# Kernel optimization log

Measured on AMD Instinct MI355X. Metric: run time of the kernel, lower is better.

## Reference

```python
import jax, jax.numpy as jnp
import numpy as np

DIM = 1024
NUM_HEADS = 16


def setup_inputs() -> dict:
    key = jax.random.key(0)
    ks = jax.random.split(key, 6)
    B, N, C = 2, 2048, DIM
    x = jax.random.normal(ks[0], (B, N, C), dtype=jnp.float32)
    # torch nn.Linear weights have shape (out, in); qkv_bias=False, proj has bias
    wq = jax.random.normal(ks[1], (C, C), dtype=jnp.float32) * 0.02
    wk = jax.random.normal(ks[2], (C, C), dtype=jnp.float32) * 0.02
    wv = jax.random.normal(ks[3], (C, C), dtype=jnp.float32) * 0.02
    wp = jax.random.normal(ks[4], (C, C), dtype=jnp.float32) * 0.02
    bp = jax.random.normal(ks[5], (C,), dtype=jnp.float32) * 0.02
    return {"x": x, "wq": wq, "wk": wk, "wv": wv, "wp": wp, "bp": bp}


def reference(x, wq, wk, wv, wp, bp):
    B, N, C = x.shape
    H = NUM_HEADS
    D = C // H
    scale = D ** (-0.5)
    # projections (torch Linear: x @ W.T), split heads -> (B, H, N, D)
    q = (x @ wq.T).reshape(B, N, H, D).transpose(0, 2, 1, 3)
    k = (x @ wk.T).reshape(B, N, H, D).transpose(0, 2, 1, 3)
    v = (x @ wv.T).reshape(B, N, H, D).transpose(0, 2, 1, 3)
    # average keys over sequence -> (B, H, D)
    k_avg = k.mean(axis=2)
    # per-position logits against the single averaged key -> (B, H, N)
    z = jnp.einsum('bhnd,bhd->bhn', q, k_avg) * scale
    attn = jax.nn.softmax(z, axis=-1)  # (B, H, N); dropout is identity at eval
    # build circulant matrix: roll_weights[..., i, j] = attn[..., (j - i) mod N]
    pos = jnp.arange(N)
    idx = (pos[None, :] - pos[:, None]) % N  # (N, N)
    roll_weights = attn[:, :, idx]  # (B, H, N, N) gather-built circulant
    out = jnp.einsum('bhij,bhjd->bhid', roll_weights, v)  # (B, H, N, D)
    out = out.transpose(0, 2, 1, 3).reshape(B, N, C)
    return out @ wp.T + bp
```

## Files before the change

### kernel.cpp

```cpp
#include <hip/hip_runtime.h>
#include <stdint.h>

typedef unsigned short u16;
typedef __bf16 bf16x8 __attribute__((ext_vector_type(8)));
typedef float f32x4 __attribute__((ext_vector_type(4)));

static constexpr int kDim   = 1024;
static constexpr int kHeads = 16;
static constexpr int kN     = 2048;
static constexpr int kB     = 2;
static constexpr int kTok   = 4096;

static constexpr size_t OFF_XB   = 0;
static constexpr size_t OFF_VT   = OFF_XB   + (size_t)kTok*kDim*2;
static constexpr size_t OFF_OC   = OFF_VT   + (size_t)kTok*kDim*2;
static constexpr size_t OFF_WVB  = OFF_OC   + (size_t)kTok*kDim*2;
static constexpr size_t OFF_WPB  = OFF_WVB  + (size_t)kDim*kDim*2;
static constexpr size_t OFF_XSUM = OFF_WPB  + (size_t)kDim*kDim*2;
static constexpr size_t OFF_KAVG = OFF_XSUM + (size_t)kB*kDim*4;
static constexpr size_t OFF_WZ   = OFF_KAVG + (size_t)kB*kHeads*64*4;
static constexpr size_t OFF_Z    = OFF_WZ   + (size_t)kB*kHeads*kDim*4;
static constexpr size_t OFF_ATTN = OFF_Z    + (size_t)kB*kHeads*kN*4;
static constexpr int kAttnStride = 2064;

__device__ __forceinline__ u16 f2bf(float f) {
  unsigned int u = __builtin_bit_cast(unsigned int, f);
  u = (u + 0x7FFFu + ((u >> 16) & 1u)) >> 16;
  return (u16)u;
}

__device__ __forceinline__ void gload_lds16(const void* g, void* l) {
  __builtin_amdgcn_global_load_lds(
      (const __attribute__((address_space(1))) unsigned int*)g,
      (__attribute__((address_space(3))) unsigned int*)l, 16, 0, 0);
}

__global__ void cvt_bf16_kernel(const float* __restrict__ in, u16* __restrict__ out, int n4) {
  int i = blockIdx.x * 256 + threadIdx.x;
  if (i < n4) {
    float4 f = reinterpret_cast<const float4*>(in)[i];
    u16 a = f2bf(f.x), b = f2bf(f.y), c = f2bf(f.z), d = f2bf(f.w);
    unsigned int lo = (unsigned int)a | ((unsigned int)b << 16);
    unsigned int hi = (unsigned int)c | ((unsigned int)d << 16);
    reinterpret_cast<uint2*>(out)[i] = make_uint2(lo, hi);
  }
}

__global__ void xsum_kernel(const float* __restrict__ x, float* __restrict__ xsum) {
  int bid = blockIdx.x;
  int cc = bid & 3, nc = (bid >> 2) & 15, b = bid >> 6;
  int c = cc * 256 + threadIdx.x;
  const float* xp = x + ((size_t)b * kN + nc * 128) * kDim + c;
  float s = 0.f;
  for (int n = 0; n < 128; ++n) s += xp[(size_t)n * kDim];
  atomicAdd(&xsum[b * kDim + c], s);
}

__global__ void kavg_kernel(const float* __restrict__ xsum, const float* __restrict__ wk,
                            float* __restrict__ kavg) {
  int o = blockIdx.x;
  int b = o >> 10;
  int lane = threadIdx.x;
  const float* wkr = wk + (size_t)(o & 1023) * kDim;
  const float* xs = xsum + b * kDim;
  float s = 0.f;
  for (int k = lane; k < kDim; k += 64) s += xs[k] * wkr[k];
#pragma unroll
  for (int off = 32; off; off >>= 1) s += __shfl_xor(s, off);
  if (lane == 0) kavg[o] = s * (1.0f / (float)kN);
}

__global__ void wz_kernel(const float* __restrict__ kavg, const float* __restrict__ wq,
                          float* __restrict__ wz) {
  int bh = blockIdx.x;
  int h = bh & 15, tid = threadIdx.x;
  __shared__ float kl[64];
  if (tid < 64) kl[tid] = kavg[bh * 64 + tid];
  __syncthreads();
  float a0 = 0.f, a1 = 0.f, a2 = 0.f, a3 = 0.f;
  const float* wqb = wq + (size_t)h * 64 * kDim + tid;
  for (int d = 0; d < 64; ++d) {
    float kd = kl[d];
    const float* r = wqb + (size_t)d * kDim;
    a0 += kd * r[0]; a1 += kd * r[256]; a2 += kd * r[512]; a3 += kd * r[768];
  }
  const float scale = 0.125f;
  float* o = wz + (size_t)bh * kDim + tid;
  o[0] = a0 * scale; o[256] = a1 * scale; o[512] = a2 * scale; o[768] = a3 * scale;
}

__global__ void z_kernel(const float* __restrict__ x, const float* __restrict__ wz,
                         float* __restrict__ z) {
  int blk = blockIdx.x;
  int b = blk >> 11, n = blk & 2047;
  __shared__ float xr[kDim];
  int tid = threadIdx.x, wid = tid >> 6, lane = tid & 63;
  reinterpret_cast<float4*>(xr)[tid] = reinterpret_cast<const float4*>(x + (size_t)blk * kDim)[tid];
  __syncthreads();
#pragma unroll
  for (int hh = 0; hh < 4; ++hh) {
    int h = wid * 4 + hh;
    const float* wzr = wz + (size_t)(b * kHeads + h) * kDim;
    float s = 0.f;
    for (int k = lane; k < kDim; k += 64) s += xr[k] * wzr[k];
#pragma unroll
    for (int off = 32; off; off >>= 1) s += __shfl_xor(s, off);
    if (lane == 0) z[(size_t)(b * kHeads + h) * kN + n] = s;
  }
}

__global__ void softmax_kernel(const float* __restrict__ z, u16* __restrict__ attn2) {
  int row = blockIdx.x, tid = threadIdx.x;
  int lane = tid & 63, wid = tid >> 6;
  const float* zr = z + (size_t)row * kN;
  float v[8];
  float mx = -1e30f;
#pragma unroll
  for (int j = 0; j < 8; ++j) { v[j] = zr[tid + j * 256]; mx = fmaxf(mx, v[j]); }
#pragma unroll
  for (int off = 32; off; off >>= 1) mx = fmaxf(mx, __shfl_xor(mx, off));
  __shared__ float redm[4], reds[4];
  if (lane == 0) redm[wid] = mx;
  __syncthreads();
  mx = fmaxf(fmaxf(redm[0], redm[1]), fmaxf(redm[2], redm[3]));
  float s = 0.f;
#pragma unroll
  for (int j = 0; j < 8; ++j) { v[j] = __expf(v[j] - mx); s += v[j]; }
#pragma unroll
  for (int off = 32; off; off >>= 1) s += __shfl_xor(s, off);
  if (lane == 0) reds[wid] = s;
  __syncthreads();
  s = reds[0] + reds[1] + reds[2] + reds[3];
  float inv = 1.0f / s;
  u16* out = attn2 + (size_t)row * kAttnStride;
#pragma unroll
  for (int j = 0; j < 8; ++j) out[tid + j * 256] = f2bf(v[j] * inv);
  if (tid < 8) out[2048 + tid] = f2bf(v[0] * inv);
}

template <int MODE>
__global__ __launch_bounds__(256, 2)
void gemm_bt_kernel(const u16* __restrict__ A, const u16* __restrict__ B,
                    void* __restrict__ Cout, const float* __restrict__ bias, int K) {
  __shared__ __align__(16) u16 As[128 * 64];
  __shared__ __align__(16) u16 Bs[64 * 64];
  int tid = threadIdx.x, lane = tid & 63, wid = tid >> 6;
  int wm = wid >> 1, wn = wid & 1;
  int lrow = lane & 15, kg = lane >> 4;
  int m0 = blockIdx.y * 128, n0 = blockIdx.x * 64;

  f32x4 acc[4][2];
#pragma unroll
  for (int i = 0; i < 4; ++i)
#pragma unroll
    for (int j = 0; j < 2; ++j) acc[i][j] = (f32x4){0.f, 0.f, 0.f, 0.f};

  for (int k0 = 0; k0 < K; k0 += 64) {
#pragma unroll
    for (int it = 0; it < 4; ++it) {
      int bchunk = it * 256 + wid * 64;
      int chunk = bchunk + lane;
      int row = chunk >> 3, cb = chunk & 7;
      int cs = cb ^ (row & 7);
      gload_lds16(A + (size_t)(m0 + row) * K + k0 + cs * 8, &As[bchunk * 8]);
    }
#pragma unroll
    for (int it = 0; it < 2; ++it) {
      int bchunk = it * 256 + wid * 64;
      int chunk = bchunk + lane;
      int row = chunk >> 3, cb = chunk & 7;
      int cs = cb ^ (row & 7);
      gload_lds16(B + (size_t)(n0 + row) * K + k0 + cs * 8, &Bs[bchunk * 8]);
    }
    __syncthreads();
#pragma unroll
    for (int ks = 0; ks < 2; ++ks) {
      bf16x8 af[4], bfv[2];
#pragma unroll
      for (int mf = 0; mf < 4; ++mf) {
        int r = wm * 64 + mf * 16 + lrow;
        int c = (ks * 4 + kg) ^ (r & 7);
        af[mf] = *reinterpret_cast<const bf16x8*>(&As[r * 64 + c * 8]);
      }
#pragma unroll
      for (int nf = 0; nf < 2; ++nf) {
        int r = wn * 32 + nf * 16 + lrow;
        int c = (ks * 4 + kg) ^ (r & 7);
        bfv[nf] = *reinterpret_cast<const bf16x8*>(&Bs[r * 64 + c * 8]);
      }
#pragma unroll
      for (int mf = 0; mf < 4; ++mf)
#pragma unroll
        for (int nf = 0; nf < 2; ++nf)
          acc[mf][nf] = __builtin_amdgcn_mfma_f32_16x16x32_bf16(af[mf], bfv[nf], acc[mf][nf], 0, 0, 0);
    }
    __syncthreads();
  }

  if (MODE == 0) {
    u16* vT = (u16*)Cout;
#pragma unroll
    for (int mf = 0; mf < 4; ++mf) {
      int row0 = m0 + wm * 64 + mf * 16 + kg * 4;
      int bb = row0 >> 11, u = row0 & 2047;
#pragma unroll
      for (int nf = 0; nf < 2; ++nf) {
        int col = n0 + wn * 32 + nf * 16 + lrow;
        f32x4 a = acc[mf][nf];
        unsigned int lo = (unsigned int)f2bf(a.x) | ((unsigned int)f2bf(a.y) << 16);
        unsigned int hi = (unsigned int)f2bf(a.z) | ((unsigned int)f2bf(a.w) << 16);
        *reinterpret_cast<uint2*>(&vT[((size_t)(bb * kDim + col)) * kN + u]) = make_uint2(lo, hi);
      }
    }
  } else {
    float* y = (float*)Cout;
#pragma unroll
    for (int nf = 0; nf < 2; ++nf) {
      int col = n0 + wn * 32 + nf * 16 + lrow;
      float bv = bias[col];
#pragma unroll
      for (int mf = 0; mf < 4; ++mf) {
        int row0 = m0 + wm * 64 + mf * 16 + kg * 4;
        f32x4 a = acc[mf][nf];
        y[(size_t)(row0 + 0) * kDim + col] = a.x + bv;
        y[(size_t)(row0 + 1) * kDim + col] = a.y + bv;
        y[(size_t)(row0 + 2) * kDim + col] = a.z + bv;
        y[(size_t)(row0 + 3) * kDim + col] = a.w + bv;
      }
    }
  }
}

__global__ __launch_bounds__(256, 2)
void conv_kernel(const u16* __restrict__ vT, const u16* __restrict__ attn2,
                 u16* __restrict__ oc) {
  static constexpr int RS = 2056;
  __shared__ __align__(16) u16 reps[8 * RS];
  __shared__ __align__(16) u16 vts[64 * 64];
  int tid = threadIdx.x, lane = tid & 63, wid = tid >> 6;
  int wm = wid >> 1, wn = wid & 1;
  int lrow = lane & 15, kg = lane >> 4;
  int i0 = blockIdx.x * 128;
  int bh = blockIdx.y;
  int b = bh >> 4, h = bh & 15;

  const u16* arow = attn2 + (size_t)bh * kAttnStride;
  for (int p = 0; p < 8; ++p)
    for (int j = tid; j < 2048; j += 256) reps[p * RS + j] = arow[j + p];

  f32x4 acc[2][4];
#pragma unroll
  for (int i = 0; i < 2; ++i)
#pragma unroll
    for (int j = 0; j < 4; ++j) acc[i][j] = (f32x4){0.f, 0.f, 0.f, 0.f};

  for (int u0 = 0; u0 < kN; u0 += 64) {
#pragma unroll
    for (int it = 0; it < 2; ++it) {
      int bchunk = it * 256 + wid * 64;
      int chunk = bchunk + lane;
      int d = chunk >> 3, cb = chunk & 7;
      int cs = cb ^ (d & 7);
      gload_lds16(vT + (size_t)(bh * 64 + d) * kN + u0 + cs * 8, &vts[bchunk * 8]);
    }
    __syncthreads();
#pragma unroll
    for (int ks = 0; ks < 2; ++ks) {
      bf16x8 af[2], bfv[4];
#pragma unroll
      for (int mf = 0; mf < 2; ++mf) {
        int r = wm * 32 + mf * 16 + lrow;
        int c = (ks * 4 + kg) ^ (r & 7);
        af[mf] = *reinterpret_cast<const bf16x8*>(&vts[r * 64 + c * 8]);
      }
#pragma unroll
      for (int nf = 0; nf < 4; ++nf) {
        int i = i0 + wn * 64 + nf * 16 + lrow;
        int s = (u0 + ks * 32 + kg * 8 - i) & 2047;
        int p = s & 7;
        bfv[nf] = *reinterpret_cast<const bf16x8*>(&reps[p * RS + (s & ~7)]);
      }
#pragma unroll
      for (int mf = 0; mf < 2; ++mf)
#pragma unroll
        for (int nf = 0; nf < 4; ++nf)
          acc[mf][nf] = __builtin_amdgcn_mfma_f32_16x16x32_bf16(af[mf], bfv[nf], acc[mf][nf], 0, 0, 0);
    }
    __syncthreads();
  }

#pragma unroll
  for (int mf = 0; mf < 2; ++mf) {
    int d = wm * 32 + mf * 16 + kg * 4;
#pragma unroll
    for (int nf = 0; nf < 4; ++nf) {
      int i = i0 + wn * 64 + nf * 16 + lrow;
      f32x4 a = acc[mf][nf];
      unsigned int lo = (unsigned int)f2bf(a.x) | ((unsigned int)f2bf(a.y) << 16);
      unsigned int hi = (unsigned int)f2bf(a.z) | ((unsigned int)f2bf(a.w) << 16);
      *reinterpret_cast<uint2*>(&oc[((size_t)(b * kN + i)) * kDim + h * 64 + d]) = make_uint2(lo, hi);
    }
  }
}

extern "C" void kernel_launch(void* const* d_in, const int* in_sizes, int n_in,
                              void* d_out, int out_size, void* d_ws, size_t ws_size,
                              hipStream_t stream) {
  const float* x  = (const float*)d_in[0];
  const float* wq = (const float*)d_in[1];
  const float* wk = (const float*)d_in[2];
  const float* wv = (const float*)d_in[3];
  const float* wp = (const float*)d_in[4];
  const float* bp = (const float*)d_in[5];
  char* ws = (char*)d_ws;

  u16*   xb    = (u16*)(ws + OFF_XB);
  u16*   vTb   = (u16*)(ws + OFF_VT);
  u16*   ocb   = (u16*)(ws + OFF_OC);
  u16*   wvb   = (u16*)(ws + OFF_WVB);
  u16*   wpb   = (u16*)(ws + OFF_WPB);
  float* xsum  = (float*)(ws + OFF_XSUM);
  float* kavg  = (float*)(ws + OFF_KAVG);
  float* wz    = (float*)(ws + OFF_WZ);
  float* z     = (float*)(ws + OFF_Z);
  u16*   attn2 = (u16*)(ws + OFF_ATTN);

  hipMemsetAsync(ws + OFF_XSUM, 0, (size_t)kB * kDim * 4, stream);

  cvt_bf16_kernel<<<4096, 256, 0, stream>>>(x,  xb,  kTok * kDim / 4);
  cvt_bf16_kernel<<<1024, 256, 0, stream>>>(wv, wvb, kDim * kDim / 4);
  cvt_bf16_kernel<<<1024, 256, 0, stream>>>(wp, wpb, kDim * kDim / 4);

  xsum_kernel<<<128, 256, 0, stream>>>(x, xsum);
  kavg_kernel<<<2048, 64, 0, stream>>>(xsum, wk, kavg);
  wz_kernel<<<32, 256, 0, stream>>>(kavg, wq, wz);
  z_kernel<<<4096, 256, 0, stream>>>(x, wz, z);
  softmax_kernel<<<32, 256, 0, stream>>>(z, attn2);

  gemm_bt_kernel<0><<<dim3(16, 32), 256, 0, stream>>>(xb, wvb, vTb, nullptr, kDim);
  conv_kernel<<<dim3(16, 32), 256, 0, stream>>>(vTb, attn2, ocb);
  gemm_bt_kernel<1><<<dim3(16, 32), 256, 0, stream>>>(ocb, wpb, (float*)d_out, bp, kDim);
}
```

Before: 210.5 us.

## Double-buffer GEMM and conv loads, enlarge GEMM tiles, fuse kavg and wz kernels

The GEMM kernel moves to 128x128 tiles with double-buffered LDS staging, so the next K-slice load overlaps MFMA work. The conv kernel gets double-buffered V tiles and a swapped grid order so blocks sharing a head run together. The kavg and wz kernels merge into one launch that reduces the key average into shared memory. Larger tiles halve the GEMM grid to 256 blocks, which may underfill the GPU, and double buffering raises LDS use per block.

```diff
diff --git a/kernel.cpp b/kernel.cpp
--- a/kernel.cpp
+++ b/kernel.cpp
@@ -17,8 +17,7 @@
 static constexpr size_t OFF_WVB  = OFF_OC   + (size_t)kTok*kDim*2;
 static constexpr size_t OFF_WPB  = OFF_WVB  + (size_t)kDim*kDim*2;
 static constexpr size_t OFF_XSUM = OFF_WPB  + (size_t)kDim*kDim*2;
-static constexpr size_t OFF_KAVG = OFF_XSUM + (size_t)kB*kDim*4;
-static constexpr size_t OFF_WZ   = OFF_KAVG + (size_t)kB*kHeads*64*4;
+static constexpr size_t OFF_WZ   = OFF_XSUM + (size_t)kB*kDim*4;
 static constexpr size_t OFF_Z    = OFF_WZ   + (size_t)kB*kHeads*kDim*4;
 static constexpr size_t OFF_ATTN = OFF_Z    + (size_t)kB*kHeads*kN*4;
 static constexpr int kAttnStride = 2064;
@@ -56,32 +55,25 @@
   atomicAdd(&xsum[b * kDim + c], s);
 }
 
-__global__ void kavg_kernel(const float* __restrict__ xsum, const float* __restrict__ wk,
-                            float* __restrict__ kavg) {
-  int o = blockIdx.x;
-  int b = o >> 10;
-  int lane = threadIdx.x;
-  const float* wkr = wk + (size_t)(o & 1023) * kDim;
+__global__ void kavgwz_kernel(const float* __restrict__ xsum, const float* __restrict__ wk,
+                              const float* __restrict__ wq, float* __restrict__ wz) {
+  int bh = blockIdx.x;
+  int b = bh >> 4, h = bh & 15, tid = threadIdx.x;
+  __shared__ float kl[64];
+  int d = tid >> 2, part = tid & 3;
+  const float* wkr = wk + (size_t)(h * 64 + d) * kDim;
   const float* xs = xsum + b * kDim;
   float s = 0.f;
-  for (int k = lane; k < kDim; k += 64) s += xs[k] * wkr[k];
-#pragma unroll
-  for (int off = 32; off; off >>= 1) s += __shfl_xor(s, off);
-  if (lane == 0) kavg[o] = s * (1.0f / (float)kN);
-}
-
-__global__ void wz_kernel(const float* __restrict__ kavg, const float* __restrict__ wq,
-                          float* __restrict__ wz) {
-  int bh = blockIdx.x;
-  int h = bh & 15, tid = threadIdx.x;
-  __shared__ float kl[64];
-  if (tid < 64) kl[tid] = kavg[bh * 64 + tid];
+  for (int k = part; k < kDim; k += 4) s += xs[k] * wkr[k];
+  s += __shfl_xor(s, 1);
+  s += __shfl_xor(s, 2);
+  if (part == 0) kl[d] = s * (1.0f / (float)kN);
   __syncthreads();
   float a0 = 0.f, a1 = 0.f, a2 = 0.f, a3 = 0.f;
   const float* wqb = wq + (size_t)h * 64 * kDim + tid;
-  for (int d = 0; d < 64; ++d) {
-    float kd = kl[d];
-    const float* r = wqb + (size_t)d * kDim;
+  for (int dd = 0; dd < 64; ++dd) {
+    float kd = kl[dd];
+    const float* r = wqb + (size_t)dd * kDim;
     a0 += kd * r[0]; a1 += kd * r[256]; a2 += kd * r[512]; a3 += kd * r[768];
   }
   const float scale = 0.125f;
@@ -142,59 +134,66 @@
 __global__ __launch_bounds__(256, 2)
 void gemm_bt_kernel(const u16* __restrict__ A, const u16* __restrict__ B,
                     void* __restrict__ Cout, const float* __restrict__ bias, int K) {
-  __shared__ __align__(16) u16 As[128 * 64];
-  __shared__ __align__(16) u16 Bs[64 * 64];
+  __shared__ __align__(16) u16 As[2][128 * 64];
+  __shared__ __align__(16) u16 Bs[2][128 * 64];
   int tid = threadIdx.x, lane = tid & 63, wid = tid >> 6;
   int wm = wid >> 1, wn = wid & 1;
   int lrow = lane & 15, kg = lane >> 4;
-  int m0 = blockIdx.y * 128, n0 = blockIdx.x * 64;
-
-  f32x4 acc[4][2];
-#pragma unroll
-  for (int i = 0; i < 4; ++i)
-#pragma unroll
-    for (int j = 0; j < 2; ++j) acc[i][j] = (f32x4){0.f, 0.f, 0.f, 0.f};
-
-  for (int k0 = 0; k0 < K; k0 += 64) {
+  int m0 = blockIdx.y * 128, n0 = blockIdx.x * 128;
+
+  auto stage = [&](int buf, int k0) {
 #pragma unroll
     for (int it = 0; it < 4; ++it) {
       int bchunk = it * 256 + wid * 64;
       int chunk = bchunk + lane;
       int row = chunk >> 3, cb = chunk & 7;
       int cs = cb ^ (row & 7);
-      gload_lds16(A + (size_t)(m0 + row) * K + k0 + cs * 8, &As[bchunk * 8]);
-    }
-#pragma unroll
-    for (int it = 0; it < 2; ++it) {
+      gload_lds16(A + (size_t)(m0 + row) * K + k0 + cs * 8, &As[buf][bchunk * 8]);
+    }
+#pragma unroll
+    for (int it = 0; it < 4; ++it) {
       int bchunk = it * 256 + wid * 64;
       int chunk = bchunk + lane;
       int row = chunk >> 3, cb = chunk & 7;
       int cs = cb ^ (row & 7);
-      gload_lds16(B + (size_t)(n0 + row) * K + k0 + cs * 8, &Bs[bchunk * 8]);
-    }
-    __syncthreads();
+      gload_lds16(B + (size_t)(n0 + row) * K + k0 + cs * 8, &Bs[buf][bchunk * 8]);
+    }
+  };
+
+  f32x4 acc[4][4];
+#pragma unroll
+  for (int i = 0; i < 4; ++i)
+#pragma unroll
+    for (int j = 0; j < 4; ++j) acc[i][j] = (f32x4){0.f, 0.f, 0.f, 0.f};
+
+  stage(0, 0);
+  __syncthreads();
+  int buf = 0;
+  for (int k0 = 0; k0 < K; k0 += 64) {
+    if (k0 + 64 < K) stage(buf ^ 1, k0 + 64);
 #pragma unroll
     for (int ks = 0; ks < 2; ++ks) {
-      bf16x8 af[4], bfv[2];
+      bf16x8 af[4], bfv[4];
 #pragma unroll
       for (int mf = 0; mf < 4; ++mf) {
         int r = wm * 64 + mf * 16 + lrow;
         int c = (ks * 4 + kg) ^ (r & 7);
-        af[mf] = *reinterpret_cast<const bf16x8*>(&As[r * 64 + c * 8]);
-      }
-#pragma unroll
-      for (int nf = 0; nf < 2; ++nf) {
-        int r = wn * 32 + nf * 16 + lrow;
+        af[mf] = *reinterpret_cast<const bf16x8*>(&As[buf][r * 64 + c * 8]);
+      }
+#pragma unroll
+      for (int nf = 0; nf < 4; ++nf) {
+        int r = wn * 64 + nf * 16 + lrow;
         int c = (ks * 4 + kg) ^ (r & 7);
-        bfv[nf] = *reinterpret_cast<const bf16x8*>(&Bs[r * 64 + c * 8]);
+        bfv[nf] = *reinterpret_cast<const bf16x8*>(&Bs[buf][r * 64 + c * 8]);
       }
 #pragma unroll
       for (int mf = 0; mf < 4; ++mf)
 #pragma unroll
-        for (int nf = 0; nf < 2; ++nf)
+        for (int nf = 0; nf < 4; ++nf)
           acc[mf][nf] = __builtin_amdgcn_mfma_f32_16x16x32_bf16(af[mf], bfv[nf], acc[mf][nf], 0, 0, 0);
     }
     __syncthreads();
+    buf ^= 1;
   }
 
   if (MODE == 0) {
@@ -204,8 +203,8 @@
       int row0 = m0 + wm * 64 + mf * 16 + kg * 4;
       int bb = row0 >> 11, u = row0 & 2047;
 #pragma unroll
-      for (int nf = 0; nf < 2; ++nf) {
-        int col = n0 + wn * 32 + nf * 16 + lrow;
+      for (int nf = 0; nf < 4; ++nf) {
+        int col = n0 + wn * 64 + nf * 16 + lrow;
         f32x4 a = acc[mf][nf];
         unsigned int lo = (unsigned int)f2bf(a.x) | ((unsigned int)f2bf(a.y) << 16);
         unsigned int hi = (unsigned int)f2bf(a.z) | ((unsigned int)f2bf(a.w) << 16);
@@ -215,8 +214,8 @@
   } else {
     float* y = (float*)Cout;
 #pragma unroll
-    for (int nf = 0; nf < 2; ++nf) {
-      int col = n0 + wn * 32 + nf * 16 + lrow;
+    for (int nf = 0; nf < 4; ++nf) {
+      int col = n0 + wn * 64 + nf * 16 + lrow;
       float bv = bias[col];
 #pragma unroll
       for (int mf = 0; mf < 4; ++mf) {
@@ -236,34 +235,40 @@
                  u16* __restrict__ oc) {
   static constexpr int RS = 2056;
   __shared__ __align__(16) u16 reps[8 * RS];
-  __shared__ __align__(16) u16 vts[64 * 64];
+  __shared__ __align__(16) u16 vts[2][64 * 64];
   int tid = threadIdx.x, lane = tid & 63, wid = tid >> 6;
   int wm = wid >> 1, wn = wid & 1;
   int lrow = lane & 15, kg = lane >> 4;
-  int i0 = blockIdx.x * 128;
-  int bh = blockIdx.y;
+  int bh = blockIdx.x;
+  int i0 = blockIdx.y * 128;
   int b = bh >> 4, h = bh & 15;
 
   const u16* arow = attn2 + (size_t)bh * kAttnStride;
   for (int p = 0; p < 8; ++p)
     for (int j = tid; j < 2048; j += 256) reps[p * RS + j] = arow[j + p];
 
-  f32x4 acc[2][4];
-#pragma unroll
-  for (int i = 0; i < 2; ++i)
-#pragma unroll
-    for (int j = 0; j < 4; ++j) acc[i][j] = (f32x4){0.f, 0.f, 0.f, 0.f};
-
-  for (int u0 = 0; u0 < kN; u0 += 64) {
+  auto stage = [&](int buf, int u0) {
 #pragma unroll
     for (int it = 0; it < 2; ++it) {
       int bchunk = it * 256 + wid * 64;
       int chunk = bchunk + lane;
       int d = chunk >> 3, cb = chunk & 7;
       int cs = cb ^ (d & 7);
-      gload_lds16(vT + (size_t)(bh * 64 + d) * kN + u0 + cs * 8, &vts[bchunk * 8]);
-    }
-    __syncthreads();
+      gload_lds16(vT + (size_t)(bh * 64 + d) * kN + u0 + cs * 8, &vts[buf][bchunk * 8]);
+    }
+  };
+
+  f32x4 acc[2][4];
+#pragma unroll
+  for (int i = 0; i < 2; ++i)
+#pragma unroll
+    for (int j = 0; j < 4; ++j) acc[i][j] = (f32x4){0.f, 0.f, 0.f, 0.f};
+
+  stage(0, 0);
+  __syncthreads();
+  int buf = 0;
+  for (int u0 = 0; u0 < kN; u0 += 64) {
+    if (u0 + 64 < kN) stage(buf ^ 1, u0 + 64);
 #pragma unroll
     for (int ks = 0; ks < 2; ++ks) {
       bf16x8 af[2], bfv[4];
@@ -271,7 +276,7 @@
       for (int mf = 0; mf < 2; ++mf) {
         int r = wm * 32 + mf * 16 + lrow;
         int c = (ks * 4 + kg) ^ (r & 7);
-        af[mf] = *reinterpret_cast<const bf16x8*>(&vts[r * 64 + c * 8]);
+        af[mf] = *reinterpret_cast<const bf16x8*>(&vts[buf][r * 64 + c * 8]);
       }
 #pragma unroll
       for (int nf = 0; nf < 4; ++nf) {
@@ -287,6 +292,7 @@
           acc[mf][nf] = __builtin_amdgcn_mfma_f32_16x16x32_bf16(af[mf], bfv[nf], acc[mf][nf], 0, 0, 0);
     }
     __syncthreads();
+    buf ^= 1;
   }
 
 #pragma unroll
@@ -320,7 +326,6 @@
   u16*   wvb   = (u16*)(ws + OFF_WVB);
   u16*   wpb   = (u16*)(ws + OFF_WPB);
   float* xsum  = (float*)(ws + OFF_XSUM);
-  float* kavg  = (float*)(ws + OFF_KAVG);
   float* wz    = (float*)(ws + OFF_WZ);
   float* z     = (float*)(ws + OFF_Z);
   u16*   attn2 = (u16*)(ws + OFF_ATTN);
@@ -332,12 +337,11 @@
   cvt_bf16_kernel<<<1024, 256, 0, stream>>>(wp, wpb, kDim * kDim / 4);
 
   xsum_kernel<<<128, 256, 0, stream>>>(x, xsum);
-  kavg_kernel<<<2048, 64, 0, stream>>>(xsum, wk, kavg);
-  wz_kernel<<<32, 256, 0, stream>>>(kavg, wq, wz);
+  kavgwz_kernel<<<32, 256, 0, stream>>>(xsum, wk, wq, wz);
   z_kernel<<<4096, 256, 0, stream>>>(x, wz, z);
   softmax_kernel<<<32, 256, 0, stream>>>(z, attn2);
 
-  gemm_bt_kernel<0><<<dim3(16, 32), 256, 0, stream>>>(xb, wvb, vTb, nullptr, kDim);
-  conv_kernel<<<dim3(16, 32), 256, 0, stream>>>(vTb, attn2, ocb);
-  gemm_bt_kernel<1><<<dim3(16, 32), 256, 0, stream>>>(ocb, wpb, (float*)d_out, bp, kDim);
-}
+  gemm_bt_kernel<0><<<dim3(8, 32), 256, 0, stream>>>(xb, wvb, vTb, nullptr, kDim);
+  conv_kernel<<<dim3(32, 16), 256, 0, stream>>>(vTb, attn2, ocb);
+  gemm_bt_kernel<1><<<dim3(8, 32), 256, 0, stream>>>(ocb, wpb, (float*)d_out, bp, kDim);
+}
```

Measured after the change: 239.5 us. +13.8%, slower.
